# Optimization experiments

Measured on AMD Instinct MI355X. Metric: run time of the kernel, lower is better.

## Reference

```python
import jax, jax.numpy as jnp
import numpy as np


def setup_inputs() -> dict:
    key = jax.random.key(0)
    ks = jax.random.split(key, 8)
    B, S, K, D = 2, 64, 64, 256
    C = D // 8
    return {
        "x": jax.random.normal(ks[0], (B, S, K, D), dtype=jnp.float32),
        "Wq": jax.random.normal(ks[1], (C, D), dtype=jnp.float32) * (1.0 / np.sqrt(D)),
        "bq": jax.random.normal(ks[2], (C,), dtype=jnp.float32) * 0.01,
        "Wk": jax.random.normal(ks[3], (C, D), dtype=jnp.float32) * (1.0 / np.sqrt(D)),
        "bk": jax.random.normal(ks[4], (C,), dtype=jnp.float32) * 0.01,
        "Wv": jax.random.normal(ks[5], (D, D), dtype=jnp.float32) * (1.0 / np.sqrt(D)),
        "bv": jax.random.normal(ks[6], (D,), dtype=jnp.float32) * 0.01,
        "gamma": jax.random.uniform(ks[7], (1,), dtype=jnp.float32),
    }


def reference(x, Wq, bq, Wk, bk, Wv, bv, gamma):
    # x: [B, S, K, D]
    B, S, K, D = x.shape
    N = K * S
    # torch: x.permute(0,3,2,1) -> [B, D, K, S]; flatten (K,S) -> N (n = k*S + s)
    xp = jnp.transpose(x, (0, 3, 2, 1)).reshape(B, D, N)  # [B, D, N]
    # 1x1 convs == per-token linear maps over the channel dim
    q = jnp.einsum('cd,bdn->bnc', Wq, xp) + bq            # [B, N, C]
    k = jnp.einsum('cd,bdn->bcn', Wk, xp) + bk[:, None]   # [B, C, N]
    energy = jnp.einsum('bnc,bcm->bnm', q, k)             # [B, N, N]
    attention = jax.nn.softmax(energy, axis=-1)           # rows sum to 1
    v = jnp.einsum('ed,bdn->ben', Wv, xp) + bv[:, None]   # [B, D, N]
    # out[b,d,i] = sum_j V[b,d,j] * A[b,i,j]
    out = jnp.einsum('bdj,bij->bdi', v, attention)        # [B, D, N]
    out = gamma * out + xp                                # residual with learned scale
    out = out.reshape(B, D, K, S)
    return jnp.transpose(out, (0, 3, 2, 1))               # [B, S, K, D]
```

## Files before the change

### kernel.cpp

```cpp
#include <hip/hip_runtime.h>
#include <stdint.h>
#include <math.h>

using short8   = __attribute__((ext_vector_type(8))) short;
using ushort4v = __attribute__((ext_vector_type(4))) unsigned short;
using f32x4    = __attribute__((ext_vector_type(4))) float;
using uint4v   = __attribute__((ext_vector_type(4))) unsigned int;
using uint2v   = __attribute__((ext_vector_type(2))) unsigned int;

#define B_ 2
#define S_ 64
#define K_ 64
#define D_ 256
#define C_ 32
#define N_ 4096
#define LOG2E 1.4426950408889634f

__device__ __forceinline__ float b2f(unsigned short u) {
    unsigned int v = ((unsigned int)u) << 16;
    return __builtin_bit_cast(float, v);
}
__device__ __forceinline__ unsigned short f2b(float f) {
    unsigned int x = __builtin_bit_cast(unsigned int, f);
    x += 0x7fffu + ((x >> 16) & 1u);
    return (unsigned short)(x >> 16);
}
__device__ __forceinline__ unsigned int pk2(float a, float b) {
    unsigned int xa = __builtin_bit_cast(unsigned int, a);
    unsigned int xb = __builtin_bit_cast(unsigned int, b);
    xa += 0x7fffu + ((xa >> 16) & 1u);
    xb += 0x7fffu + ((xb >> 16) & 1u);
    return (xa >> 16) | (xb & 0xffff0000u);
}

__global__ __launch_bounds__(256) void wcvt_kernel(
    const float* __restrict__ Wq, const float* __restrict__ bq,
    const float* __restrict__ Wk, const float* __restrict__ bk,
    const float* __restrict__ Wv, const float* __restrict__ bv,
    unsigned short* __restrict__ Wh, unsigned short* __restrict__ Wl,
    float* __restrict__ bcat)
{
    int oc = blockIdx.x;
    int d  = threadIdx.x;
    float w;
    if (oc < 32)       w = Wq[oc * 256 + d] * LOG2E;
    else if (oc < 64)  w = Wk[(oc - 32) * 256 + d];
    else               w = Wv[(oc - 64) * 256 + d];
    unsigned short h = f2b(w);
    Wh[oc * 256 + d] = h;
    Wl[oc * 256 + d] = f2b(w - b2f(h));
    if (d == 0) {
        float bb;
        if (oc < 32)      bb = bq[oc] * LOG2E;
        else if (oc < 64) bb = bk[oc - 32];
        else              bb = bv[oc - 64];
        bcat[oc] = bb;
    }
}

__global__ __launch_bounds__(256) void qkv_kernel(
    const float* __restrict__ x,
    const unsigned short* __restrict__ Wh, const unsigned short* __restrict__ Wl,
    const float* __restrict__ bcat,
    unsigned short* __restrict__ Qh, unsigned short* __restrict__ Ql,
    unsigned short* __restrict__ Kh, unsigned short* __restrict__ Kl,
    unsigned short* __restrict__ Vm)
{
    __shared__ unsigned short lxh[16 * 256];
    __shared__ unsigned short lxl[16 * 256];

    int tid = threadIdx.x;
    int bid = blockIdx.x;
    int b  = bid >> 8;
    int n0 = (bid & 255) << 4;

    {
        int tt = tid >> 4, dg0 = (tid & 15) * 16;
        int n = n0 + tt;
        int s = n & 63, kk = n >> 6;
        const float* xr = x + (((size_t)(b * S_ + s)) * K_ + kk) * D_ + dg0;
        short8 h0, l0, h1, l1;
#pragma unroll
        for (int e = 0; e < 8; ++e) {
            float v = xr[e];
            unsigned short hh = f2b(v);
            h0[e] = (short)hh; l0[e] = (short)f2b(v - b2f(hh));
        }
#pragma unroll
        for (int e = 0; e < 8; ++e) {
            float v = xr[8 + e];
            unsigned short hh = f2b(v);
            h1[e] = (short)hh; l1[e] = (short)f2b(v - b2f(hh));
        }
        int m0 = dg0 >> 3;
        int sw0 = ((m0 ^ (tt & 7)) << 3);
        int sw1 = (((m0 + 1) ^ (tt & 7)) << 3);
        *(short8*)(lxh + tt * 256 + sw0) = h0;
        *(short8*)(lxh + tt * 256 + sw1) = h1;
        *(short8*)(lxl + tt * 256 + sw0) = l0;
        *(short8*)(lxl + tt * 256 + sw1) = l1;
    }
    __syncthreads();

    int wave = tid >> 6, lane = tid & 63;
    int col = lane & 15, g = lane >> 4;

#pragma unroll
    for (int i = 0; i < 5; ++i) {
        int ct = wave + i * 4;
        int oc0 = ct * 16;
        const unsigned short* whr = Wh + (size_t)(oc0 + col) * 256;
        const unsigned short* wlr = Wl + (size_t)(oc0 + col) * 256;
        f32x4 acc = {0.f, 0.f, 0.f, 0.f};

        if (ct < 4) {
#pragma unroll
            for (int dc = 0; dc < 8; ++dc) {
                int sw = (((dc * 4 + g) ^ (col & 7)) << 3);
                short8 xh8 = *(const short8*)(lxh + col * 256 + sw);
                short8 xl8 = *(const short8*)(lxl + col * 256 + sw);
                short8 wh8 = *(const short8*)(whr + dc * 32 + g * 8);
                short8 wl8 = *(const short8*)(wlr + dc * 32 + g * 8);
                acc = __builtin_amdgcn_mfma_f32_16x16x32_bf16(xl8, wh8, acc, 0, 0, 0);
                acc = __builtin_amdgcn_mfma_f32_16x16x32_bf16(xh8, wl8, acc, 0, 0, 0);
                acc = __builtin_amdgcn_mfma_f32_16x16x32_bf16(xh8, wh8, acc, 0, 0, 0);
            }
            float bb = bcat[oc0 + col];
            unsigned short* Th = (ct < 2) ? Qh : Kh;
            unsigned short* Tl = (ct < 2) ? Ql : Kl;
            int c0 = (ct & 1) * 16;
#pragma unroll
            for (int r = 0; r < 4; ++r) {
                int tok = n0 + g * 4 + r;
                float v = acc[r] + bb;
                unsigned short hh = f2b(v);
                size_t idx = ((size_t)b * N_ + tok) * C_ + c0 + col;
                Th[idx] = hh;
                Tl[idx] = f2b(v - b2f(hh));
            }
        } else {
#pragma unroll
            for (int dc = 0; dc < 8; ++dc) {
                int sw = (((dc * 4 + g) ^ (col & 7)) << 3);
                short8 xh8 = *(const short8*)(lxh + col * 256 + sw);
                short8 wh8 = *(const short8*)(whr + dc * 32 + g * 8);
                acc = __builtin_amdgcn_mfma_f32_16x16x32_bf16(xh8, wh8, acc, 0, 0, 0);
            }
            float bb = bcat[oc0 + col];
            int c0 = oc0 - 64;
            ushort4v st;
#pragma unroll
            for (int r = 0; r < 4; ++r) st[r] = f2b(acc[r] + bb);
            int tok0 = n0 + g * 4;
            int s0 = 8 * g + ((n0 & 16) >> 2);
            int d_ch = c0 + col;
            int o = d_ch * 64 + s0 * 2;
            o ^= (d_ch & 7) << 4;
            size_t vbyteoff = ((size_t)b * (N_ / 32) + (tok0 >> 5)) * (D_ * 32 * 2)
                            + (size_t)o;
            *(ushort4v*)((char*)Vm + vbyteoff) = st;
        }
    }
}

__global__ __launch_bounds__(1024, 4) void attn_kernel(
    const unsigned short* __restrict__ Qh, const unsigned short* __restrict__ Ql,
    const unsigned short* __restrict__ Kh, const unsigned short* __restrict__ Kl,
    const unsigned short* __restrict__ Vm,
    unsigned short* __restrict__ O_bf16, float* __restrict__ lsum_part)
{
    __shared__ __align__(16) char vlds[2][16384];
    __shared__ __align__(16) char plds[2 * 8192];

    int tid  = threadIdx.x;
    int wave = tid >> 6;
    int lane = tid & 63;
    int col = lane & 15, g = lane >> 4;
    int qq = wave >> 2;
    int dq = wave & 3;
    int kh = dq & 1;
    int qs_own = dq >> 1;
    int tid16 = tid * 16;
    int lane16 = lane * 16;

    int bid = blockIdx.x;
    int x7 = bid & 7;
    int b  = x7 >> 2;
    int ks = x7 & 3;
    int qt = bid >> 3;
    int q0 = qt * 128 + qq * 32;
    int jbase = ks * (N_ / 4);

    size_t qoff = ((size_t)b * N_ + q0 + qs_own * 16 + col) * C_ + g * 8;
    short8 qfh = *(const short8*)(Qh + qoff);
    short8 qfl = *(const short8*)(Ql + qoff);

    f32x4 acc[2][4];
#pragma unroll
    for (int qs = 0; qs < 2; ++qs)
#pragma unroll
        for (int dt = 0; dt < 4; ++dt) acc[qs][dt] = (f32x4){0.f, 0.f, 0.f, 0.f};
    float l_run = 0.f;

    const unsigned short* kbh = Kh + (size_t)b * N_ * C_;
    const unsigned short* kbl = Kl + (size_t)b * N_ * C_;
    const char* vbyte = (const char*)Vm + (size_t)b * ((size_t)N_ * D_ * 2);

    auto kaddr = [&](int it) {
        return (size_t)(jbase + it * 32 + kh * 16 + col) * C_ + g * 8;
    };

    unsigned vro = (unsigned)(((dq * 64 + col) * 64 + g * 16) ^ ((col & 7) << 4));
    int st = qq * 2 + qs_own;
    char* pmy = plds + st * 1024 + lane16 + kh * 8;
    const char* pr0 = plds + (qq * 2) * 1024 + lane16;
    const char* pr1 = plds + (qq * 2 + 1) * 1024 + lane16;

    {
        const char* vsrc = vbyte + (size_t)(ks * 32) * 16384 + tid16;
        *(f32x4*)(vlds[0] + tid16) = *(const f32x4*)(vsrc);
    }
    short8 khA = *(const short8*)(kbh + kaddr(0));
    short8 klA = *(const short8*)(kbl + kaddr(0));
    short8 khB = *(const short8*)(kbh + kaddr(1));
    short8 klB = *(const short8*)(kbl + kaddr(1));
    {
        f32x4 z = {0.f, 0.f, 0.f, 0.f};
        f32x4 sa = __builtin_amdgcn_mfma_f32_16x16x32_bf16(klA, qfh, z, 0, 0, 0);
        sa = __builtin_amdgcn_mfma_f32_16x16x32_bf16(khA, qfl, sa, 0, 0, 0);
        sa = __builtin_amdgcn_mfma_f32_16x16x32_bf16(khA, qfh, sa, 0, 0, 0);
        float pa[4];
#pragma unroll
        for (int r = 0; r < 4; ++r) pa[r] = exp2f(sa[r]);
        l_run += (pa[0] + pa[1]) + (pa[2] + pa[3]);
        uint2v uo;
        uo[0] = pk2(pa[0], pa[1]); uo[1] = pk2(pa[2], pa[3]);
        *(uint2v*)(pmy) = uo;
    }
    __syncthreads();

#define ATTN_PHASE(IT, CKH, CKL, NKH, NKL)                                       \
    {                                                                            \
        int itn_ = (IT) + 1;                                                     \
        int itk_ = (IT) + 2;         \
        const char* vsrc_ = vbyte + (size_t)(ks * 32 + itn_) * 16384 + tid16;    \
        f32x4 stg_ = *(const f32x4*)(vsrc_);                                     \
        NKH = *(const short8*)(kbh + kaddr(itk_));                               \
        NKL = *(const short8*)(kbl + kaddr(itk_));                               \
        __builtin_amdgcn_sched_barrier(0);        \
        f32x4 z_ = {0.f, 0.f, 0.f, 0.f};                                         \
        __builtin_amdgcn_s_setprio(1);                                           \
        f32x4 sa_ = __builtin_amdgcn_mfma_f32_16x16x32_bf16(CKL, qfh, z_, 0, 0, 0); \
        sa_ = __builtin_amdgcn_mfma_f32_16x16x32_bf16(CKH, qfl, sa_, 0, 0, 0);   \
        sa_ = __builtin_amdgcn_mfma_f32_16x16x32_bf16(CKH, qfh, sa_, 0, 0, 0);   \
        __builtin_amdgcn_s_setprio(0);                                           \
        float pa_[4];                                                            \
        _Pragma("unroll")                                                        \
        for (int r = 0; r < 4; ++r) pa_[r] = exp2f(sa_[r]);                      \
        l_run += (pa_[0] + pa_[1]) + (pa_[2] + pa_[3]);                          \
        uint2v uo_;                                                              \
        uo_[0] = pk2(pa_[0], pa_[1]); uo_[1] = pk2(pa_[2], pa_[3]);              \
        int rb_ = (IT) & 1, wb_ = (itn_) & 1;                                    \
        short8 pf0_ = *(const short8*)(pr0 + rb_ * 8192);                        \
        short8 pf1_ = *(const short8*)(pr1 + rb_ * 8192);                        \
        short8 vf_[4];                                                           \
        _Pragma("unroll")                                                        \
        for (int dt = 0; dt < 4; ++dt)                                           \
            vf_[dt] = *(const short8*)(vlds[rb_] + vro + dt * 1024);             \
        __builtin_amdgcn_s_setprio(1);                                           \
        _Pragma("unroll")                                                        \
        for (int dt = 0; dt < 4; ++dt) {                                         \
            acc[0][dt] = __builtin_amdgcn_mfma_f32_16x16x32_bf16(vf_[dt], pf0_, acc[0][dt], 0, 0, 0); \
            acc[1][dt] = __builtin_amdgcn_mfma_f32_16x16x32_bf16(vf_[dt], pf1_, acc[1][dt], 0, 0, 0); \
        }                                                                        \
        __builtin_amdgcn_s_setprio(0);                                           \
        *(uint2v*)(pmy + wb_ * 8192) = uo_;                                      \
        *(f32x4*)(vlds[wb_] + tid16) = stg_;                                     \
        __syncthreads();                                                         \
    }

    for (int it2 = 0; it2 < 15; ++it2) {
        int itA = it2 * 2, itB = itA + 1;
        ATTN_PHASE(itA, khB, klB, khA, klA);
        ATTN_PHASE(itB, khA, klA, khB, klB);
    }
    ATTN_PHASE(30, khB, klB, khA, klA);
#undef ATTN_PHASE

    {
        short8 pf0 = *(const short8*)(pr0 + 8192);
        short8 pf1 = *(const short8*)(pr1 + 8192);
        short8 vf[4];
#pragma unroll
        for (int dt = 0; dt < 4; ++dt)
            vf[dt] = *(const short8*)(vlds[1] + vro + dt * 1024);
#pragma unroll
        for (int dt = 0; dt < 4; ++dt) {
            acc[0][dt] = __builtin_amdgcn_mfma_f32_16x16x32_bf16(vf[dt], pf0, acc[0][dt], 0, 0, 0);
            acc[1][dt] = __builtin_amdgcn_mfma_f32_16x16x32_bf16(vf[dt], pf1, acc[1][dt], 0, 0, 0);
        }
    }

    l_run += __shfl_xor(l_run, 16); l_run += __shfl_xor(l_run, 32);

    unsigned short* op = O_bf16 + (size_t)bid * 32768 + (qq * 2 + (dq >> 1)) * 4096;
#pragma unroll
    for (int qs = 0; qs < 2; ++qs)
#pragma unroll
        for (int dt = 0; dt < 4; ++dt) {
            int j = qs * 8 + (dq & 1) * 4 + dt;
            uint2v uo;
            uo[0] = pk2(acc[qs][dt][0], acc[qs][dt][1]);
            uo[1] = pk2(acc[qs][dt][2], acc[qs][dt][3]);
            *(uint2v*)(op + j * 256 + col * 16 + g * 4) = uo;
        }
    if (g == 0)
        lsum_part[bid * 256 + kh * 128 + qq * 32 + qs_own * 16 + col] = l_run;
}

__global__ __launch_bounds__(256) void epi_kernel(
    const unsigned short* __restrict__ O_bf16, const float* __restrict__ lsum_part,
    const float* __restrict__ x, const float* __restrict__ gamma_p,
    float* __restrict__ out)
{
    int gid = blockIdx.x * 256 + threadIdx.x;
    int d  = (gid & 63) * 4;
    int nl = gid >> 6;
    int b  = nl >> 12;
    int n  = nl & (N_ - 1);

    int qt = n >> 7, qq = (n >> 5) & 3, qs = (n >> 4) & 1, col = n & 15;
    int dh = d >> 7, dt = (d >> 4) & 7;
    int w = qq * 2 + dh, j = qs * 8 + dt;
    int boff = w * 4096 + j * 256 + col * 16 + (d & 15);
    int loff = qq * 32 + qs * 16 + col;

    f32x4 acc = {0.f, 0.f, 0.f, 0.f};
    float l = 0.f;
#pragma unroll
    for (int ks = 0; ks < 4; ++ks) {
        int bid = qt * 8 + b * 4 + ks;
        ushort4v p = *(const ushort4v*)(O_bf16 + (size_t)bid * 32768 + boff);
        acc[0] += b2f(p[0]); acc[1] += b2f(p[1]);
        acc[2] += b2f(p[2]); acc[3] += b2f(p[3]);
        l += lsum_part[bid * 256 + loff] + lsum_part[bid * 256 + 128 + loff];
    }
    float scale = gamma_p[0] / l;
    int s = n & 63, kk = n >> 6;
    size_t o = (((size_t)(b * S_ + s)) * K_ + kk) * D_ + d;
    f32x4 xv = *(const f32x4*)(x + o);
    f32x4 ov;
#pragma unroll
    for (int e = 0; e < 4; ++e) ov[e] = acc[e] * scale + xv[e];
    *(f32x4*)(out + o) = ov;
}

extern "C" void kernel_launch(void* const* d_in, const int* in_sizes, int n_in,
                              void* d_out, int out_size, void* d_ws, size_t ws_size,
                              hipStream_t stream) {
    const float* x  = (const float*)d_in[0];
    const float* Wq = (const float*)d_in[1];
    const float* bq = (const float*)d_in[2];
    const float* Wk = (const float*)d_in[3];
    const float* bk = (const float*)d_in[4];
    const float* Wv = (const float*)d_in[5];
    const float* bv = (const float*)d_in[6];
    const float* gm = (const float*)d_in[7];

    char* ws = (char*)d_ws;
    unsigned short* Wh   = (unsigned short*)(ws);
    unsigned short* Wl   = (unsigned short*)(ws + 0x40000);
    float*          bcat = (float*)         (ws + 0x80000);
    unsigned short* Qh   = (unsigned short*)(ws + 0x100000);
    unsigned short* Ql   = (unsigned short*)(ws + 0x180000);
    unsigned short* Kh   = (unsigned short*)(ws + 0x200000);
    unsigned short* Kl   = (unsigned short*)(ws + 0x280000);
    unsigned short* Vm   = (unsigned short*)(ws + 0x300000);
    unsigned short* Op   = (unsigned short*)(ws + 0x700000);
    float*          lp   = (float*)         (ws + 0x2700000);
    float* o = (float*)d_out;

    wcvt_kernel<<<320, 256, 0, stream>>>(Wq, bq, Wk, bk, Wv, bv, Wh, Wl, bcat);
    qkv_kernel<<<512, 256, 0, stream>>>(x, Wh, Wl, bcat, Qh, Ql, Kh, Kl, Vm);
    attn_kernel<<<256, 1024, 0, stream>>>(Qh, Ql, Kh, Kl, Vm, Op, lp);
    epi_kernel<<<2048, 256, 0, stream>>>(Op, lp, x, gm, o);
}
```

Baseline: 62.97 us.

## Stage V tiles via direct global-to-LDS loads and widen qkv blocks to 512 threads

In the attention kernel, the V tile prefetch now uses global_load_lds to write straight into the LDS double buffer, removing the register staging and the separate LDS store. In the qkv kernel, blocks grow to 512 threads: four waves handle the split-precision Q/K projection while four other waves each compute four V channel tiles, and each thread converts half as many x elements. The direct LDS write is issued earlier and relies on the existing barrier for ordering, which could create a race on the buffer if the async write is not waited on before reads.

```diff
diff --git a/kernel.cpp b/kernel.cpp
--- a/kernel.cpp
+++ b/kernel.cpp
@@ -31,6 +31,11 @@
     xa += 0x7fffu + ((xa >> 16) & 1u);
     xb += 0x7fffu + ((xb >> 16) & 1u);
     return (xa >> 16) | (xb & 0xffff0000u);
+}
+__device__ __forceinline__ void gld_lds16(const void* g, void* l) {
+    __builtin_amdgcn_global_load_lds(
+        (const __attribute__((address_space(1))) unsigned int*)g,
+        (__attribute__((address_space(3))) unsigned int*)l, 16, 0, 0);
 }
 
 __global__ __launch_bounds__(256) void wcvt_kernel(
@@ -58,7 +63,7 @@
     }
 }
 
-__global__ __launch_bounds__(256) void qkv_kernel(
+__global__ __launch_bounds__(512) void qkv_kernel(
     const float* __restrict__ x,
     const unsigned short* __restrict__ Wh, const unsigned short* __restrict__ Wl,
     const float* __restrict__ bcat,
@@ -75,70 +80,64 @@
     int n0 = (bid & 255) << 4;
 
     {
-        int tt = tid >> 4, dg0 = (tid & 15) * 16;
+        int tt = tid >> 5, m = tid & 31;
         int n = n0 + tt;
         int s = n & 63, kk = n >> 6;
-        const float* xr = x + (((size_t)(b * S_ + s)) * K_ + kk) * D_ + dg0;
-        short8 h0, l0, h1, l1;
+        const float* xr = x + (((size_t)(b * S_ + s)) * K_ + kk) * D_ + m * 8;
+        short8 h8, l8;
 #pragma unroll
         for (int e = 0; e < 8; ++e) {
             float v = xr[e];
             unsigned short hh = f2b(v);
-            h0[e] = (short)hh; l0[e] = (short)f2b(v - b2f(hh));
-        }
-#pragma unroll
-        for (int e = 0; e < 8; ++e) {
-            float v = xr[8 + e];
-            unsigned short hh = f2b(v);
-            h1[e] = (short)hh; l1[e] = (short)f2b(v - b2f(hh));
-        }
-        int m0 = dg0 >> 3;
-        int sw0 = ((m0 ^ (tt & 7)) << 3);
-        int sw1 = (((m0 + 1) ^ (tt & 7)) << 3);
-        *(short8*)(lxh + tt * 256 + sw0) = h0;
-        *(short8*)(lxh + tt * 256 + sw1) = h1;
-        *(short8*)(lxl + tt * 256 + sw0) = l0;
-        *(short8*)(lxl + tt * 256 + sw1) = l1;
+            h8[e] = (short)hh; l8[e] = (short)f2b(v - b2f(hh));
+        }
+        int sw = ((m ^ (tt & 7)) << 3);
+        *(short8*)(lxh + tt * 256 + sw) = h8;
+        *(short8*)(lxl + tt * 256 + sw) = l8;
     }
     __syncthreads();
 
     int wave = tid >> 6, lane = tid & 63;
     int col = lane & 15, g = lane >> 4;
 
-#pragma unroll
-    for (int i = 0; i < 5; ++i) {
-        int ct = wave + i * 4;
+    if (wave < 4) {
+        int ct = wave;
         int oc0 = ct * 16;
         const unsigned short* whr = Wh + (size_t)(oc0 + col) * 256;
         const unsigned short* wlr = Wl + (size_t)(oc0 + col) * 256;
         f32x4 acc = {0.f, 0.f, 0.f, 0.f};
-
-        if (ct < 4) {
-#pragma unroll
-            for (int dc = 0; dc < 8; ++dc) {
-                int sw = (((dc * 4 + g) ^ (col & 7)) << 3);
-                short8 xh8 = *(const short8*)(lxh + col * 256 + sw);
-                short8 xl8 = *(const short8*)(lxl + col * 256 + sw);
-                short8 wh8 = *(const short8*)(whr + dc * 32 + g * 8);
-                short8 wl8 = *(const short8*)(wlr + dc * 32 + g * 8);
-                acc = __builtin_amdgcn_mfma_f32_16x16x32_bf16(xl8, wh8, acc, 0, 0, 0);
-                acc = __builtin_amdgcn_mfma_f32_16x16x32_bf16(xh8, wl8, acc, 0, 0, 0);
-                acc = __builtin_amdgcn_mfma_f32_16x16x32_bf16(xh8, wh8, acc, 0, 0, 0);
-            }
-            float bb = bcat[oc0 + col];
-            unsigned short* Th = (ct < 2) ? Qh : Kh;
-            unsigned short* Tl = (ct < 2) ? Ql : Kl;
-            int c0 = (ct & 1) * 16;
-#pragma unroll
-            for (int r = 0; r < 4; ++r) {
-                int tok = n0 + g * 4 + r;
-                float v = acc[r] + bb;
-                unsigned short hh = f2b(v);
-                size_t idx = ((size_t)b * N_ + tok) * C_ + c0 + col;
-                Th[idx] = hh;
-                Tl[idx] = f2b(v - b2f(hh));
-            }
-        } else {
+#pragma unroll
+        for (int dc = 0; dc < 8; ++dc) {
+            int sw = (((dc * 4 + g) ^ (col & 7)) << 3);
+            short8 xh8 = *(const short8*)(lxh + col * 256 + sw);
+            short8 xl8 = *(const short8*)(lxl + col * 256 + sw);
+            short8 wh8 = *(const short8*)(whr + dc * 32 + g * 8);
+            short8 wl8 = *(const short8*)(wlr + dc * 32 + g * 8);
+            acc = __builtin_amdgcn_mfma_f32_16x16x32_bf16(xl8, wh8, acc, 0, 0, 0);
+            acc = __builtin_amdgcn_mfma_f32_16x16x32_bf16(xh8, wl8, acc, 0, 0, 0);
+            acc = __builtin_amdgcn_mfma_f32_16x16x32_bf16(xh8, wh8, acc, 0, 0, 0);
+        }
+        float bb = bcat[oc0 + col];
+        unsigned short* Th = (ct < 2) ? Qh : Kh;
+        unsigned short* Tl = (ct < 2) ? Ql : Kl;
+        int c0 = (ct & 1) * 16;
+#pragma unroll
+        for (int r = 0; r < 4; ++r) {
+            int tok = n0 + g * 4 + r;
+            float v = acc[r] + bb;
+            unsigned short hh = f2b(v);
+            size_t idx = ((size_t)b * N_ + tok) * C_ + c0 + col;
+            Th[idx] = hh;
+            Tl[idx] = f2b(v - b2f(hh));
+        }
+    } else {
+        int i = wave - 4;
+#pragma unroll
+        for (int k = 0; k < 4; ++k) {
+            int ct = 4 + i + 4 * k;
+            int oc0 = ct * 16;
+            const unsigned short* whr = Wh + (size_t)(oc0 + col) * 256;
+            f32x4 acc = {0.f, 0.f, 0.f, 0.f};
 #pragma unroll
             for (int dc = 0; dc < 8; ++dc) {
                 int sw = (((dc * 4 + g) ^ (col & 7)) << 3);
@@ -216,10 +215,7 @@
     const char* pr0 = plds + (qq * 2) * 1024 + lane16;
     const char* pr1 = plds + (qq * 2 + 1) * 1024 + lane16;
 
-    {
-        const char* vsrc = vbyte + (size_t)(ks * 32) * 16384 + tid16;
-        *(f32x4*)(vlds[0] + tid16) = *(const f32x4*)(vsrc);
-    }
+    gld_lds16(vbyte + (size_t)(ks * 32) * 16384 + tid16, vlds[0] + tid16);
     short8 khA = *(const short8*)(kbh + kaddr(0));
     short8 klA = *(const short8*)(kbl + kaddr(0));
     short8 khB = *(const short8*)(kbh + kaddr(1));
@@ -243,8 +239,9 @@
     {                                                                            \
         int itn_ = (IT) + 1;                                                     \
         int itk_ = (IT) + 2;         \
-        const char* vsrc_ = vbyte + (size_t)(ks * 32 + itn_) * 16384 + tid16;    \
-        f32x4 stg_ = *(const f32x4*)(vsrc_);                                     \
+        int rb_ = (IT) & 1, wb_ = (itn_) & 1;                                    \
+        gld_lds16(vbyte + (size_t)(ks * 32 + itn_) * 16384 + tid16,              \
+                  vlds[wb_] + tid16);                                            \
         NKH = *(const short8*)(kbh + kaddr(itk_));                               \
         NKL = *(const short8*)(kbl + kaddr(itk_));                               \
         __builtin_amdgcn_sched_barrier(0);        \
@@ -260,7 +257,6 @@
         l_run += (pa_[0] + pa_[1]) + (pa_[2] + pa_[3]);                          \
         uint2v uo_;                                                              \
         uo_[0] = pk2(pa_[0], pa_[1]); uo_[1] = pk2(pa_[2], pa_[3]);              \
-        int rb_ = (IT) & 1, wb_ = (itn_) & 1;                                    \
         short8 pf0_ = *(const short8*)(pr0 + rb_ * 8192);                        \
         short8 pf1_ = *(const short8*)(pr1 + rb_ * 8192);                        \
         short8 vf_[4];                                                           \
@@ -275,7 +271,6 @@
         }                                                                        \
         __builtin_amdgcn_s_setprio(0);                                           \
         *(uint2v*)(pmy + wb_ * 8192) = uo_;                                      \
-        *(f32x4*)(vlds[wb_] + tid16) = stg_;                                     \
         __syncthreads();                                                         \
     }
 
@@ -381,7 +376,7 @@
     float* o = (float*)d_out;
 
     wcvt_kernel<<<320, 256, 0, stream>>>(Wq, bq, Wk, bk, Wv, bv, Wh, Wl, bcat);
-    qkv_kernel<<<512, 256, 0, stream>>>(x, Wh, Wl, bcat, Qh, Ql, Kh, Kl, Vm);
+    qkv_kernel<<<512, 512, 0, stream>>>(x, Wh, Wl, bcat, Qh, Ql, Kh, Kl, Vm);
     attn_kernel<<<256, 1024, 0, stream>>>(Qh, Ql, Kh, Kl, Vm, Op, lp);
     epi_kernel<<<2048, 256, 0, stream>>>(Op, lp, x, gm, o);
 }
```

Result: slower. 67.05 us (+6.5%).
